# Performance work log

Hardware: AMD Instinct MI355X
Metric: run time of the kernel (lower is better)

## Reference

```python
import jax, jax.numpy as jnp
import numpy as np

C, D, H, Z, B = 10, 3072, 512, 256, 2048  # classes, img_dim, hidden, latent, batch


def setup_inputs() -> dict:
    key = jax.random.key(0)
    ks = jax.random.split(key, 8)
    def w(k, shape, fan_in):
        return jax.random.normal(k, shape, jnp.float32) * (1.0 / np.sqrt(fan_in)).astype(np.float32)
    return {
        "img": jax.random.normal(ks[0], (B, D), jnp.float32),
        "label": jax.random.randint(ks[1], (B,), 0, C, dtype=jnp.int32),
        "enc_w1": w(ks[2], (C, D, H), D), "enc_b1": jnp.zeros((C, H), jnp.float32),
        "enc_w2": w(ks[3], (C, H, Z), H), "enc_b2": jnp.zeros((C, Z), jnp.float32),
        "dec_w1": w(ks[4], (C, Z, H), Z), "dec_b1": jnp.zeros((C, H), jnp.float32),
        "dec_w2": w(ks[5], (C, H, D), H), "dec_b2": jnp.zeros((C, D), jnp.float32),
    }


def reference(img, label, enc_w1, enc_b1, enc_w2, enc_b2,
              dec_w1, dec_b1, dec_w2, dec_b2):
    # Label-conditioned dispatch: rows with label==c go through expert c's
    # encoder-decoder; outputs scattered back into a zero-initialized image.
    # Loop is over a small fixed class count (structurally distinct experts);
    # masked-select via jnp.where is mathematically identical to the
    # gather/scatter in the torch code (absent classes contribute nothing).
    out_img = jnp.zeros_like(img)
    n_classes = enc_w1.shape[0]
    for c in range(n_classes):
        h = jax.nn.relu(img @ enc_w1[c] + enc_b1[c])       # [B,H]
        z = h @ enc_w2[c] + enc_b2[c]                      # [B,Z] latent code
        h2 = jax.nn.relu(z @ dec_w1[c] + dec_b1[c])        # [B,H]
        y = h2 @ dec_w2[c] + dec_b2[c]                     # [B,D]
        out_img = jnp.where((label == c)[:, None], y, out_img)
    loss = jnp.mean((out_img - img) ** 2)
    return loss, out_img
```

## Files before the change

kernel.cpp:

```cpp
#include <hip/hip_runtime.h>
#include <hip/hip_bf16.h>

#define C_CLS 10
#define DIM   3072
#define HID   512
#define LAT   256
#define BATCH 2048
#define BM    64
#define GRID_TILES 42

typedef __attribute__((ext_vector_type(8))) short  s16x8;
typedef __attribute__((ext_vector_type(4))) float  f32x4;
typedef __attribute__((ext_vector_type(8))) __bf16 bf16x8;

struct Meta {
    int offsets[C_CLS + 1];
    int ntiles;
    int tileClass[GRID_TILES];
    int tileRow[GRID_TILES];
    int perm[BATCH];
};

__device__ __forceinline__ unsigned short f2bf(float f) {
    unsigned u = __builtin_bit_cast(unsigned, f);
    unsigned r = (u + 0x7fffu + ((u >> 16) & 1u)) >> 16;
    return (unsigned short)r;
}

__device__ __forceinline__ f32x4 mfma16(s16x8 a, s16x8 b, f32x4 c) {
    return __builtin_amdgcn_mfma_f32_16x16x32_bf16(
        __builtin_bit_cast(bf16x8, a), __builtin_bit_cast(bf16x8, b), c, 0, 0, 0);
}

__global__ __launch_bounds__(256) void setup_kernel(const int* __restrict__ label,
                                                    Meta* __restrict__ mt,
                                                    float* __restrict__ out) {
    __shared__ int h[C_CLS];
    __shared__ int loff[C_CLS + 1];
    int tid = threadIdx.x;
    if (tid < C_CLS) h[tid] = 0;
    __syncthreads();
    for (int i = tid; i < BATCH; i += 256) atomicAdd(&h[label[i]], 1);
    __syncthreads();
    if (tid == 0) {
        int s = 0, nt = 0;
        for (int c = 0; c < C_CLS; ++c) { loff[c] = s; s += h[c]; }
        loff[C_CLS] = s;
        for (int c = 0; c < C_CLS; ++c) {
            mt->offsets[c] = loff[c];
            int cnt = h[c];
            for (int t = 0; t < cnt; t += BM) {
                mt->tileClass[nt] = c;
                mt->tileRow[nt]   = loff[c] + t;
                ++nt;
            }
            h[c] = loff[c];
        }
        mt->offsets[C_CLS] = loff[C_CLS];
        mt->ntiles = nt;
        out[0] = 0.0f;
    }
    __syncthreads();
    for (int i = tid; i < BATCH; i += 256) {
        int pos = atomicAdd(&h[label[i]], 1);
        mt->perm[pos] = i;
    }
}

template <int KTOT, int KSPLIT, int N, int NPART, bool RELUIN, bool FINAL>
__global__ __launch_bounds__(256) void gemm_kernel(const float* __restrict__ Ain,
                                                   const float* __restrict__ abias,
                                                   const float* __restrict__ W,
                                                   const float* __restrict__ obias,
                                                   float* __restrict__ Pout,
                                                   float* __restrict__ outF,
                                                   const float* __restrict__ img,
                                                   const Meta* __restrict__ mt) {
    int ty = blockIdx.y;
    if (ty >= mt->ntiles) return;
    const int c     = mt->tileClass[ty];
    const int r0    = mt->tileRow[ty];
    const int rend  = mt->offsets[c + 1];
    const int n0    = blockIdx.x * 64;
    const int kbase = blockIdx.z * (KTOT / KSPLIT);
    constexpr int NT = KTOT / KSPLIT / 64;

    const float* Wc = W + (size_t)c * KTOT * N + n0;

    __shared__ __align__(16) unsigned short As[2][64 * 64];
    __shared__ __align__(16) unsigned short Bs[2][64 * 64];

    const int tid  = threadIdx.x;
    const int lane = tid & 63;
    const int wid  = tid >> 6;
    const int wm   = wid >> 1, wn = wid & 1;

    const int aRow0 = tid >> 3;
    const int aSlot = tid & 7;
    const int bO    = tid >> 5;
    const int bN2   = tid & 31;

    constexpr int NP = (NPART == 0) ? 1 : NPART;
    float4 ga[NP][2][2];
    float4 gbias[2];
    float2 bb[8];

    auto load_tile = [&](int k0) {
#pragma unroll
        for (int h = 0; h < 2; ++h) {
            int row = aRow0 + h * 32;
            int ar  = min(r0 + row, rend - 1);
            if constexpr (NPART == 0) {
                int orig = mt->perm[ar];
                const float* src = Ain + (size_t)orig * KTOT + k0 + aSlot * 8;
                ga[0][h][0] = *(const float4*)(src);
                ga[0][h][1] = *(const float4*)(src + 4);
            } else {
#pragma unroll
                for (int p = 0; p < NP; ++p) {
                    const float* src = Ain + ((size_t)p * BATCH + ar) * KTOT + k0 + aSlot * 8;
                    ga[p][h][0] = *(const float4*)(src);
                    ga[p][h][1] = *(const float4*)(src + 4);
                }
            }
        }
        if constexpr (NPART > 0) {
            const float* bsrc = abias + (size_t)c * KTOT + k0 + aSlot * 8;
            gbias[0] = *(const float4*)(bsrc);
            gbias[1] = *(const float4*)(bsrc + 4);
        }
        const float* src = Wc + (size_t)(k0 + 8 * bO) * N + 2 * bN2;
#pragma unroll
        for (int i = 0; i < 8; ++i) bb[i] = *(const float2*)(src + (size_t)i * N);
    };

    auto write_tile = [&](int buf) {
#pragma unroll
        for (int h = 0; h < 2; ++h) {
            int row = aRow0 + h * 32;
            s16x8 v;
#pragma unroll
            for (int q = 0; q < 2; ++q)
#pragma unroll
                for (int j = 0; j < 4; ++j) {
                    float s;
                    if constexpr (NPART == 0) {
                        s = ((const float*)&ga[0][h][q])[j];
                    } else {
                        s = ((const float*)&gbias[q])[j];
#pragma unroll
                        for (int p = 0; p < NP; ++p) s += ((const float*)&ga[p][h][q])[j];
                        if (RELUIN) s = fmaxf(s, 0.0f);
                    }
                    ((unsigned short*)&v)[q * 4 + j] = f2bf(s);
                }
            *(s16x8*)(&As[buf][row * 64 + ((aSlot ^ (row & 7))) * 8]) = v;
        }
#pragma unroll
        for (int nn = 0; nn < 2; ++nn) {
            int n = 2 * bN2 + nn;
            s16x8 v;
#pragma unroll
            for (int i = 0; i < 8; ++i)
                ((unsigned short*)&v)[i] = f2bf(nn ? bb[i].y : bb[i].x);
            *(s16x8*)(&Bs[buf][n * 64 + ((bO ^ (n & 7))) * 8]) = v;
        }
    };

    f32x4 acc[2][2] = {};

    load_tile(kbase);
    write_tile(0);
    __syncthreads();

    for (int t = 0; t < NT; ++t) {
        int cur = t & 1;
        if (t + 1 < NT) load_tile(kbase + (t + 1) * 64);
#pragma unroll
        for (int ks = 0; ks < 2; ++ks) {
            int kslot = ks * 4 + (lane >> 4);
            int rA0 = wm * 32 + (lane & 15), rA1 = rA0 + 16;
            int rB0 = wn * 32 + (lane & 15), rB1 = rB0 + 16;
            s16x8 a0 = *(const s16x8*)(&As[cur][rA0 * 64 + (kslot ^ (rA0 & 7)) * 8]);
            s16x8 a1 = *(const s16x8*)(&As[cur][rA1 * 64 + (kslot ^ (rA1 & 7)) * 8]);
            s16x8 b0 = *(const s16x8*)(&Bs[cur][rB0 * 64 + (kslot ^ (rB0 & 7)) * 8]);
            s16x8 b1 = *(const s16x8*)(&Bs[cur][rB1 * 64 + (kslot ^ (rB1 & 7)) * 8]);
            acc[0][0] = mfma16(a0, b0, acc[0][0]);
            acc[0][1] = mfma16(a0, b1, acc[0][1]);
            acc[1][0] = mfma16(a1, b0, acc[1][0]);
            acc[1][1] = mfma16(a1, b1, acc[1][1]);
        }
        if (t + 1 < NT) write_tile(cur ^ 1);
        __syncthreads();
    }

    const int col = lane & 15;
    const int rq  = lane >> 4;
    if constexpr (!FINAL) {
        float* P = Pout + (size_t)blockIdx.z * BATCH * N;
#pragma unroll
        for (int mi = 0; mi < 2; ++mi)
#pragma unroll
            for (int ni = 0; ni < 2; ++ni) {
                int n = n0 + wn * 32 + ni * 16 + col;
#pragma unroll
                for (int r = 0; r < 4; ++r) {
                    int m = r0 + wm * 32 + mi * 16 + rq * 4 + r;
                    if (m < rend) P[(size_t)m * N + n] = acc[mi][ni][r];
                }
            }
    } else {
        float lsum = 0.0f;
#pragma unroll
        for (int mi = 0; mi < 2; ++mi) {
#pragma unroll
            for (int r = 0; r < 4; ++r) {
                int m = r0 + wm * 32 + mi * 16 + rq * 4 + r;
                if (m < rend) {
                    int orig = mt->perm[m];
#pragma unroll
                    for (int ni = 0; ni < 2; ++ni) {
                        int n   = n0 + wn * 32 + ni * 16 + col;
                        float v = acc[mi][ni][r] + obias[(size_t)c * N + n];
                        size_t idx = (size_t)orig * N + n;
                        outF[1 + idx] = v;
                        float d = v - img[idx];
                        lsum += d * d;
                    }
                }
            }
        }
#pragma unroll
        for (int o = 32; o > 0; o >>= 1) lsum += __shfl_down(lsum, o);
        __shared__ float red[4];
        if (lane == 0) red[wid] = lsum;
        __syncthreads();
        if (tid == 0)
            atomicAdd(&outF[0],
                      (red[0] + red[1] + red[2] + red[3]) * (1.0f / ((float)BATCH * (float)DIM)));
    }
}

extern "C" void kernel_launch(void* const* d_in, const int* in_sizes, int n_in,
                              void* d_out, int out_size, void* d_ws, size_t ws_size,
                              hipStream_t stream) {
    const float* img    = (const float*)d_in[0];
    const int*   label  = (const int*)d_in[1];
    const float* enc_w1 = (const float*)d_in[2];
    const float* enc_b1 = (const float*)d_in[3];
    const float* enc_w2 = (const float*)d_in[4];
    const float* enc_b2 = (const float*)d_in[5];
    const float* dec_w1 = (const float*)d_in[6];
    const float* dec_b1 = (const float*)d_in[7];
    const float* dec_w2 = (const float*)d_in[8];
    const float* dec_b2 = (const float*)d_in[9];
    float* out = (float*)d_out;

    auto alignup = [](size_t x) { return (x + 255) & ~(size_t)255; };
    char* p = (char*)d_ws;
    size_t off = 0;
    Meta* meta = (Meta*)p;                  off += alignup(sizeof(Meta));
    float* P1  = (float*)(p + off);         off += alignup((size_t)4 * BATCH * HID * 4);
    float* PZ  = (float*)(p + off);         off += alignup((size_t)4 * BATCH * LAT * 4);
    float* PH2 = (float*)(p + off);         off += alignup((size_t)2 * BATCH * HID * 4);
    (void)ws_size; (void)in_sizes; (void)n_in; (void)out_size;

    setup_kernel<<<1, 256, 0, stream>>>(label, meta, out);

    gemm_kernel<DIM, 4, HID, 0, false, false><<<dim3(HID / 64, GRID_TILES, 4), 256, 0, stream>>>(
        img, nullptr, enc_w1, nullptr, P1, nullptr, nullptr, meta);
    gemm_kernel<HID, 4, LAT, 4, true, false><<<dim3(LAT / 64, GRID_TILES, 4), 256, 0, stream>>>(
        P1, enc_b1, enc_w2, nullptr, PZ, nullptr, nullptr, meta);
    gemm_kernel<LAT, 2, HID, 4, false, false><<<dim3(HID / 64, GRID_TILES, 2), 256, 0, stream>>>(
        PZ, enc_b2, dec_w1, nullptr, PH2, nullptr, nullptr, meta);
    gemm_kernel<HID, 1, DIM, 2, true, true><<<dim3(DIM / 64, GRID_TILES, 1), 256, 0, stream>>>(
        PH2, dec_b1, dec_w2, dec_b2, nullptr, out, img, meta);
}
```

Before: 303.6 us.

## Pre-gather bf16 activations and reduce split-K partials in separate kernels

```diff
diff --git a/kernel.cpp b/kernel.cpp
--- a/kernel.cpp
+++ b/kernel.cpp
@@ -19,6 +19,7 @@
     int tileClass[GRID_TILES];
     int tileRow[GRID_TILES];
     int perm[BATCH];
+    int rowcls[BATCH];
 };
 
 __device__ __forceinline__ unsigned short f2bf(float f) {
@@ -62,20 +63,66 @@
     }
     __syncthreads();
     for (int i = tid; i < BATCH; i += 256) {
-        int pos = atomicAdd(&h[label[i]], 1);
-        mt->perm[pos] = i;
-    }
-}
-
-template <int KTOT, int KSPLIT, int N, int NPART, bool RELUIN, bool FINAL>
-__global__ __launch_bounds__(256) void gemm_kernel(const float* __restrict__ Ain,
-                                                   const float* __restrict__ abias,
+        int lb  = label[i];
+        int pos = atomicAdd(&h[lb], 1);
+        mt->perm[pos]   = i;
+        mt->rowcls[pos] = lb;
+    }
+}
+
+__global__ __launch_bounds__(256) void gather_kernel(const float* __restrict__ img,
+                                                     const Meta* __restrict__ mt,
+                                                     unsigned short* __restrict__ Xg) {
+    int p    = blockIdx.x;
+    int orig = mt->perm[p];
+    const float4* src = (const float4*)(img + (size_t)orig * DIM);
+    unsigned short* dst = Xg + (size_t)p * DIM;
+    for (int j = threadIdx.x; j < DIM / 4; j += 256) {
+        float4 v = src[j];
+        unsigned short o[4] = {f2bf(v.x), f2bf(v.y), f2bf(v.z), f2bf(v.w)};
+        *(uint2*)(dst + 4 * j) = *(const uint2*)o;
+    }
+}
+
+template <int N, int KS, bool RELU>
+__global__ __launch_bounds__(256) void reduce_kernel(const float* __restrict__ P,
+                                                     const float* __restrict__ bias,
+                                                     const Meta* __restrict__ mt,
+                                                     unsigned short* __restrict__ out) {
+    int idx = blockIdx.x * 256 + threadIdx.x;
+    int p   = idx / (N / 8);
+    int n8  = idx - p * (N / 8);
+    const float* b = bias + (size_t)mt->rowcls[p] * N + n8 * 8;
+    f32x4 s0 = *(const f32x4*)(b);
+    f32x4 s1 = *(const f32x4*)(b + 4);
+#pragma unroll
+    for (int ks = 0; ks < KS; ++ks) {
+        const float* src = P + ((size_t)ks * BATCH + p) * N + n8 * 8;
+        s0 += *(const f32x4*)(src);
+        s1 += *(const f32x4*)(src + 4);
+    }
+    s16x8 v;
+#pragma unroll
+    for (int j = 0; j < 4; ++j) {
+        float a = s0[j], c = s1[j];
+        if (RELU) { a = fmaxf(a, 0.0f); c = fmaxf(c, 0.0f); }
+        ((unsigned short*)&v)[j]     = f2bf(a);
+        ((unsigned short*)&v)[4 + j] = f2bf(c);
+    }
+    *(s16x8*)(out + (size_t)p * N + n8 * 8) = v;
+}
+
+template <int KTOT, int KSPLIT, int N, bool FINAL>
+__global__ __launch_bounds__(256) void gemm_kernel(const unsigned short* __restrict__ Ain,
                                                    const float* __restrict__ W,
                                                    const float* __restrict__ obias,
                                                    float* __restrict__ Pout,
                                                    float* __restrict__ outF,
                                                    const float* __restrict__ img,
                                                    const Meta* __restrict__ mt) {
+    constexpr int NT = KTOT / KSPLIT / 64;
+    static_assert(NT >= 2 && (NT % 2) == 0, "NT must be even and >= 2");
+
     int ty = blockIdx.y;
     if (ty >= mt->ntiles) return;
     const int c     = mt->tileClass[ty];
@@ -83,7 +130,6 @@
     const int rend  = mt->offsets[c + 1];
     const int n0    = blockIdx.x * 64;
     const int kbase = blockIdx.z * (KTOT / KSPLIT);
-    constexpr int NT = KTOT / KSPLIT / 64;
 
     const float* Wc = W + (size_t)c * KTOT * N + n0;
 
@@ -100,61 +146,26 @@
     const int bO    = tid >> 5;
     const int bN2   = tid & 31;
 
-    constexpr int NP = (NPART == 0) ? 1 : NPART;
-    float4 ga[NP][2][2];
-    float4 gbias[2];
-    float2 bb[8];
-
-    auto load_tile = [&](int k0) {
-#pragma unroll
-        for (int h = 0; h < 2; ++h) {
-            int row = aRow0 + h * 32;
-            int ar  = min(r0 + row, rend - 1);
-            if constexpr (NPART == 0) {
-                int orig = mt->perm[ar];
-                const float* src = Ain + (size_t)orig * KTOT + k0 + aSlot * 8;
-                ga[0][h][0] = *(const float4*)(src);
-                ga[0][h][1] = *(const float4*)(src + 4);
-            } else {
-#pragma unroll
-                for (int p = 0; p < NP; ++p) {
-                    const float* src = Ain + ((size_t)p * BATCH + ar) * KTOT + k0 + aSlot * 8;
-                    ga[p][h][0] = *(const float4*)(src);
-                    ga[p][h][1] = *(const float4*)(src + 4);
-                }
-            }
-        }
-        if constexpr (NPART > 0) {
-            const float* bsrc = abias + (size_t)c * KTOT + k0 + aSlot * 8;
-            gbias[0] = *(const float4*)(bsrc);
-            gbias[1] = *(const float4*)(bsrc + 4);
-        }
+    struct Stage { s16x8 a0, a1; float2 b[8]; };
+    Stage s0, s1;
+
+    const int ar0 = min(r0 + aRow0, rend - 1);
+    const int ar1 = min(r0 + aRow0 + 32, rend - 1);
+
+    auto load_stage = [&](Stage& S, int k0) {
+        S.a0 = *(const s16x8*)(Ain + (size_t)ar0 * KTOT + k0 + aSlot * 8);
+        S.a1 = *(const s16x8*)(Ain + (size_t)ar1 * KTOT + k0 + aSlot * 8);
         const float* src = Wc + (size_t)(k0 + 8 * bO) * N + 2 * bN2;
 #pragma unroll
-        for (int i = 0; i < 8; ++i) bb[i] = *(const float2*)(src + (size_t)i * N);
+        for (int i = 0; i < 8; ++i) S.b[i] = *(const float2*)(src + (size_t)i * N);
     };
 
-    auto write_tile = [&](int buf) {
-#pragma unroll
-        for (int h = 0; h < 2; ++h) {
-            int row = aRow0 + h * 32;
-            s16x8 v;
-#pragma unroll
-            for (int q = 0; q < 2; ++q)
-#pragma unroll
-                for (int j = 0; j < 4; ++j) {
-                    float s;
-                    if constexpr (NPART == 0) {
-                        s = ((const float*)&ga[0][h][q])[j];
-                    } else {
-                        s = ((const float*)&gbias[q])[j];
-#pragma unroll
-                        for (int p = 0; p < NP; ++p) s += ((const float*)&ga[p][h][q])[j];
-                        if (RELUIN) s = fmaxf(s, 0.0f);
-                    }
-                    ((unsigned short*)&v)[q * 4 + j] = f2bf(s);
-                }
-            *(s16x8*)(&As[buf][row * 64 + ((aSlot ^ (row & 7))) * 8]) = v;
+    auto write_stage = [&](const Stage& S, int buf) {
+        {
+            int row = aRow0;
+            *(s16x8*)(&As[buf][row * 64 + ((aSlot ^ (row & 7))) * 8]) = S.a0;
+            row = aRow0 + 32;
+            *(s16x8*)(&As[buf][row * 64 + ((aSlot ^ (row & 7))) * 8]) = S.a1;
         }
 #pragma unroll
         for (int nn = 0; nn < 2; ++nn) {
@@ -162,35 +173,43 @@
             s16x8 v;
 #pragma unroll
             for (int i = 0; i < 8; ++i)
-                ((unsigned short*)&v)[i] = f2bf(nn ? bb[i].y : bb[i].x);
+                ((unsigned short*)&v)[i] = f2bf(nn ? S.b[i].y : S.b[i].x);
             *(s16x8*)(&Bs[buf][n * 64 + ((bO ^ (n & 7))) * 8]) = v;
         }
     };
 
     f32x4 acc[2][2] = {};
 
-    load_tile(kbase);
-    write_tile(0);
-    __syncthreads();
-
-    for (int t = 0; t < NT; ++t) {
-        int cur = t & 1;
-        if (t + 1 < NT) load_tile(kbase + (t + 1) * 64);
+    auto compute = [&](int buf) {
 #pragma unroll
         for (int ks = 0; ks < 2; ++ks) {
             int kslot = ks * 4 + (lane >> 4);
             int rA0 = wm * 32 + (lane & 15), rA1 = rA0 + 16;
             int rB0 = wn * 32 + (lane & 15), rB1 = rB0 + 16;
-            s16x8 a0 = *(const s16x8*)(&As[cur][rA0 * 64 + (kslot ^ (rA0 & 7)) * 8]);
-            s16x8 a1 = *(const s16x8*)(&As[cur][rA1 * 64 + (kslot ^ (rA1 & 7)) * 8]);
-            s16x8 b0 = *(const s16x8*)(&Bs[cur][rB0 * 64 + (kslot ^ (rB0 & 7)) * 8]);
-            s16x8 b1 = *(const s16x8*)(&Bs[cur][rB1 * 64 + (kslot ^ (rB1 & 7)) * 8]);
+            s16x8 a0 = *(const s16x8*)(&As[buf][rA0 * 64 + (kslot ^ (rA0 & 7)) * 8]);
+            s16x8 a1 = *(const s16x8*)(&As[buf][rA1 * 64 + (kslot ^ (rA1 & 7)) * 8]);
+            s16x8 b0 = *(const s16x8*)(&Bs[buf][rB0 * 64 + (kslot ^ (rB0 & 7)) * 8]);
+            s16x8 b1 = *(const s16x8*)(&Bs[buf][rB1 * 64 + (kslot ^ (rB1 & 7)) * 8]);
             acc[0][0] = mfma16(a0, b0, acc[0][0]);
             acc[0][1] = mfma16(a0, b1, acc[0][1]);
             acc[1][0] = mfma16(a1, b0, acc[1][0]);
             acc[1][1] = mfma16(a1, b1, acc[1][1]);
         }
-        if (t + 1 < NT) write_tile(cur ^ 1);
+    };
+
+    load_stage(s0, kbase);
+    load_stage(s1, kbase + 64);
+    write_stage(s0, 0);
+    __syncthreads();
+
+    for (int t = 0; t < NT; t += 2) {
+        if (t + 2 < NT) load_stage(s0, kbase + (t + 2) * 64);
+        compute(0);
+        if (t + 1 < NT) write_stage(s1, 1);
+        __syncthreads();
+        if (t + 3 < NT) load_stage(s1, kbase + (t + 3) * 64);
+        compute(1);
+        if (t + 2 < NT) write_stage(s0, 0);
         __syncthreads();
     }
 
@@ -259,20 +278,31 @@
     auto alignup = [](size_t x) { return (x + 255) & ~(size_t)255; };
     char* p = (char*)d_ws;
     size_t off = 0;
-    Meta* meta = (Meta*)p;                  off += alignup(sizeof(Meta));
-    float* P1  = (float*)(p + off);         off += alignup((size_t)4 * BATCH * HID * 4);
-    float* PZ  = (float*)(p + off);         off += alignup((size_t)4 * BATCH * LAT * 4);
-    float* PH2 = (float*)(p + off);         off += alignup((size_t)2 * BATCH * HID * 4);
+    Meta* meta = (Meta*)p;                           off += alignup(sizeof(Meta));
+    float* P1  = (float*)(p + off);                  off += alignup((size_t)4 * BATCH * HID * 4);
+    float* P2  = (float*)(p + off);                  off += alignup((size_t)4 * BATCH * LAT * 4);
+    float* P3  = (float*)(p + off);                  off += alignup((size_t)2 * BATCH * HID * 4);
+    unsigned short* Xg = (unsigned short*)(p + off); off += alignup((size_t)BATCH * DIM * 2);
+    unsigned short* H1 = (unsigned short*)(p + off); off += alignup((size_t)BATCH * HID * 2);
+    unsigned short* Zb = (unsigned short*)(p + off); off += alignup((size_t)BATCH * LAT * 2);
+    unsigned short* H2 = (unsigned short*)(p + off); off += alignup((size_t)BATCH * HID * 2);
     (void)ws_size; (void)in_sizes; (void)n_in; (void)out_size;
 
     setup_kernel<<<1, 256, 0, stream>>>(label, meta, out);
-
-    gemm_kernel<DIM, 4, HID, 0, false, false><<<dim3(HID / 64, GRID_TILES, 4), 256, 0, stream>>>(
-        img, nullptr, enc_w1, nullptr, P1, nullptr, nullptr, meta);
-    gemm_kernel<HID, 4, LAT, 4, true, false><<<dim3(LAT / 64, GRID_TILES, 4), 256, 0, stream>>>(
-        P1, enc_b1, enc_w2, nullptr, PZ, nullptr, nullptr, meta);
-    gemm_kernel<LAT, 2, HID, 4, false, false><<<dim3(HID / 64, GRID_TILES, 2), 256, 0, stream>>>(
-        PZ, enc_b2, dec_w1, nullptr, PH2, nullptr, nullptr, meta);
-    gemm_kernel<HID, 1, DIM, 2, true, true><<<dim3(DIM / 64, GRID_TILES, 1), 256, 0, stream>>>(
-        PH2, dec_b1, dec_w2, dec_b2, nullptr, out, img, meta);
-}
+    gather_kernel<<<BATCH, 256, 0, stream>>>(img, meta, Xg);
+
+    gemm_kernel<DIM, 4, HID, false><<<dim3(HID / 64, GRID_TILES, 4), 256, 0, stream>>>(
+        Xg, enc_w1, nullptr, P1, nullptr, nullptr, meta);
+    reduce_kernel<HID, 4, true><<<BATCH * HID / 2048, 256, 0, stream>>>(P1, enc_b1, meta, H1);
+
+    gemm_kernel<HID, 4, LAT, false><<<dim3(LAT / 64, GRID_TILES, 4), 256, 0, stream>>>(
+        H1, enc_w2, nullptr, P2, nullptr, nullptr, meta);
+    reduce_kernel<LAT, 4, false><<<BATCH * LAT / 2048, 256, 0, stream>>>(P2, enc_b2, meta, Zb);
+
+    gemm_kernel<LAT, 2, HID, false><<<dim3(HID / 64, GRID_TILES, 2), 256, 0, stream>>>(
+        Zb, dec_w1, nullptr, P3, nullptr, nullptr, meta);
+    reduce_kernel<HID, 2, true><<<BATCH * HID / 2048, 256, 0, stream>>>(P3, dec_b1, meta, H2);
+
+    gemm_kernel<HID, 1, DIM, true><<<dim3(DIM / 64, GRID_TILES, 1), 256, 0, stream>>>(
+        H2, dec_w2, dec_b2, nullptr, out, img, meta);
+}
```

New measurement: 277.5 us. 8.6% less time.
